# Performance work log

Measured on AMD Instinct MI355X. Metric: run time of the kernel, lower is better.

The kernel has to match this reference:

```python
import jax, jax.numpy as jnp
import numpy as np
from jax import lax

START_IDX = 0
STOP_IDX = 1


def _forward_alg(feats_lbt, mask_lb, transitions):
    # feats_lbt: [L, B, T], mask_lb: [L, B], transitions[i, j] = score(j -> i)
    L, B, T = feats_lbt.shape
    init = jnp.full((B, T), -10000.0, dtype=feats_lbt.dtype).at[:, START_IDX].set(0.0)

    def step(fv, xs):
        feat, m = xs  # feat: [B, T], m: [B]
        # scores[b, next, prev] = fv[b, prev] + transitions[next, prev] + feat[b, next]
        scores = fv[:, None, :] + transitions[None, :, :] + feat[:, :, None]
        alphas = jax.nn.logsumexp(scores, axis=-1)  # [B, T]
        fv = jnp.where(m[:, None] > 0, alphas, fv)
        return fv, None

    fv, _ = lax.scan(step, init, (feats_lbt, mask_lb))
    terminal = fv + transitions[STOP_IDX][None, :]
    return jax.nn.logsumexp(terminal, axis=-1)  # [B]


def _score_sentence(feats_lbt, tags_bl, mask_lb, transitions):
    L, B, T = feats_lbt.shape
    start_col = jnp.full((B, 1), START_IDX, dtype=tags_bl.dtype)
    tags_ext = jnp.concatenate([start_col, tags_bl], axis=-1)  # [B, L+1]
    # transition scores along the gold path: [B, L]
    trans = transitions[tags_ext[:, 1:], tags_ext[:, :-1]]
    # emission scores: feats is [L, B, T] -> gather per-position gold tag
    emit = jnp.take_along_axis(
        feats_lbt, tags_bl.T[:, :, None], axis=-1
    )[:, :, 0]  # [L, B]
    step_scores = (trans.T + emit) * (mask_lb > 0)  # [L, B]
    score = step_scores.sum(axis=0)  # [B]
    lengths = mask_lb.sum(axis=0).astype(jnp.int32)  # [B]
    last_tag = tags_ext[jnp.arange(B), lengths]
    score = score + transitions[STOP_IDX, last_tag]
    return score


def setup_inputs() -> dict:
    key = jax.random.key(0)
    k1, k2, k3 = jax.random.split(key, 3)
    B, L, T = 256, 2048, 32
    efeats = jax.random.normal(k1, (B, L, T), dtype=jnp.float32)
    mask = jnp.ones((B, L), dtype=jnp.float32)
    tgt = jax.random.randint(k2, (B, L), 0, T, dtype=jnp.int32)
    transitions = jax.random.normal(k3, (T, T), dtype=jnp.float32)
    return {"efeats": efeats, "mask": mask, "tgt": tgt, "transitions": transitions}


def reference(efeats, mask, tgt, transitions):
    B, L = mask.shape
    mask_lb = mask.T  # [L, B]
    feats_lbt = jnp.transpose(efeats, (1, 0, 2))  # [L, B, T]
    forward_score = _forward_alg(feats_lbt, mask_lb, transitions)
    gold_score = _score_sentence(feats_lbt, tgt, mask_lb, transitions)
    loss = (forward_score - gold_score).sum() / B
    return loss
```

## Files before the change

kernel.cpp:

```cpp
#include <hip/hip_runtime.h>

#define B_SZ 256
#define L_SZ 2048
#define T_SZ 32
#define START_IDX 0
#define STOP_IDX 1

#define CLEN 64
#define NCHB 8
#define NCH_SEQ 32
#define NBLK_SEQ 4
#define NBLK_TOT (B_SZ * NBLK_SEQ)

#define FB_NCH 16
#define FB_CLEN 128

typedef __attribute__((ext_vector_type(8))) short bf16x8;
typedef __attribute__((ext_vector_type(4))) float f32x4;
typedef __attribute__((ext_vector_type(2))) float f32x2;

__device__ __forceinline__ unsigned fau(float f){ union{float f; unsigned u;} v; v.f=f; return v.u; }
__device__ __forceinline__ float uaf(unsigned u){ union{unsigned u; float f;} v; v.u=u; return v.f; }
__device__ __forceinline__ int pack_trunc(float lo, float hi){
  return (int)__builtin_amdgcn_perm(fau(hi), fau(lo), 0x07060302u);
}
__device__ __forceinline__ bf16x8 frag_of(const int* p){
  union{ int i[4]; bf16x8 v; } u;
  u.i[0]=p[0]; u.i[1]=p[1]; u.i[2]=p[2]; u.i[3]=p[3];
  return u.v;
}

__global__ void zero_kernel(float* out){ if(threadIdx.x==0) out[0]=0.f; }

__device__ __forceinline__ int mat_prod(const unsigned short* L, const unsigned short* Rt,
                                        unsigned short* dst, bool writeT, int lane)
{
  const int g = lane >> 4, c16 = lane & 15;
  const int ko = 8*g;
  bf16x8 A0 = *(const bf16x8*)(L  + (c16*T_SZ      + ko));
  bf16x8 A1 = *(const bf16x8*)(L  + ((16+c16)*T_SZ + ko));
  bf16x8 B0 = *(const bf16x8*)(Rt + (c16*T_SZ      + ko));
  bf16x8 B1 = *(const bf16x8*)(Rt + ((16+c16)*T_SZ + ko));
  const f32x4 zf = {0.f,0.f,0.f,0.f};
  f32x4 q00 = __builtin_amdgcn_mfma_f32_16x16x32_bf16(A0, B0, zf, 0,0,0);
  f32x4 q01 = __builtin_amdgcn_mfma_f32_16x16x32_bf16(A0, B1, zf, 0,0,0);
  f32x4 q10 = __builtin_amdgcn_mfma_f32_16x16x32_bf16(A1, B0, zf, 0,0,0);
  f32x4 q11 = __builtin_amdgcn_mfma_f32_16x16x32_bf16(A1, B1, zf, 0,0,0);

  unsigned mb = (unsigned)__builtin_amdgcn_readfirstlane((int)fau(q00[0]));
  int e = (int)((mb>>23)&255u) - 127;
  float r = uaf((unsigned)(127-e)<<23);
  #pragma unroll
  for (int i=0;i<4;++i){ q00[i]*=r; q01[i]*=r; q10[i]*=r; q11[i]*=r; }

  if (!writeT){
    #pragma unroll
    for (int reg=0; reg<4; ++reg){
      int x0 = 4*g + reg, x1 = 16 + 4*g + reg;
      dst[x0*T_SZ + c16]      = (unsigned short)(fau(q00[reg])>>16);
      dst[x0*T_SZ + 16 + c16] = (unsigned short)(fau(q01[reg])>>16);
      dst[x1*T_SZ + c16]      = (unsigned short)(fau(q10[reg])>>16);
      dst[x1*T_SZ + 16 + c16] = (unsigned short)(fau(q11[reg])>>16);
    }
  } else {
    #pragma unroll
    for (int rp=0; rp<2; ++rp){
      int xb0 = 4*g + 2*rp, xb1 = 16 + 4*g + 2*rp;
      *(int*)&dst[c16*T_SZ + xb0]        = pack_trunc(q00[2*rp], q00[2*rp+1]);
      *(int*)&dst[(16+c16)*T_SZ + xb0]   = pack_trunc(q01[2*rp], q01[2*rp+1]);
      *(int*)&dst[c16*T_SZ + xb1]        = pack_trunc(q10[2*rp], q10[2*rp+1]);
      *(int*)&dst[(16+c16)*T_SZ + xb1]   = pack_trunc(q11[2*rp], q11[2*rp+1]);
    }
  }
  return e;
}

__global__ __launch_bounds__(512, 6) void crf_chunk_kernel(
    const float* __restrict__ efeats, const float* __restrict__ mask,
    const int* __restrict__ tgt, const float* __restrict__ trans,
    unsigned short* __restrict__ wsM, int* __restrict__ wsE,
    float* __restrict__ wsG, float* __restrict__ wsL)
{
  __shared__ float s_trans[T_SZ*T_SZ];
  __shared__ float s_d[NCHB][128];
  __shared__ unsigned short s_tree[NCHB][T_SZ*T_SZ];
  __shared__ int   s_et[NCHB];
  __shared__ float s_gd[NCHB], s_ml[NCHB];

  const int tid  = threadIdx.x;
  const int w    = tid >> 6;
  const int lane = tid & 63;
  const int g    = lane >> 4;
  const int c16  = lane & 15;

  const int b  = blockIdx.x >> 2;
  const int q  = blockIdx.x & 3;
  const int c  = q*NCHB + w;
  const int l0 = c * CLEN;

  s_trans[tid]     = trans[tid];
  s_trans[tid+512] = trans[tid+512];
  __syncthreads();

  int a0[4], a1[4];
  #pragma unroll
  for (int I=0; I<2; ++I){
    int row = 8*(c16>>2) + 4*I + (c16&3);
    float e[8];
    #pragma unroll
    for (int j=0;j<8;++j) e[j] = __expf(s_trans[row*T_SZ + 8*g + j]);
    int* dst = I ? a1 : a0;
    #pragma unroll
    for (int p=0;p<4;++p) dst[p] = pack_trunc(e[2*p], e[2*p+1]);
  }

  int b0[4], b1[4];
  #pragma unroll
  for (int p=0;p<4;++p){
    int s0 = 8*g + 2*p, s1 = s0+1;
    unsigned lo = (s0==c16)?0x3f80u:0u, hi = (s1==c16)?0x3f80u:0u;
    b0[p] = (int)(lo | (hi<<16));
    lo = (s0==16+c16)?0x3f80u:0u; hi = (s1==16+c16)?0x3f80u:0u;
    b1[p] = (int)(lo | (hi<<16));
  }

  const long fbase = ((long)b * L_SZ) * T_SZ;
  const int  mbase = b*L_SZ + l0;

  float maskv = mask[mbase + lane];
  int   tcur  = tgt [mbase + lane];
  int   tprev;
  {
    int lp = (l0 + lane == 0) ? mbase : (mbase + lane - 1);
    tprev = tgt[lp];
    if (l0 + lane == 0) tprev = START_IDX;
  }

  float emitg = efeats[fbase + (long)(l0+lane)*T_SZ + tcur];
  float gl = (maskv > 0.f) ? (s_trans[tcur*T_SZ + tprev] + emitg) : 0.f;
  float ml = maskv;
  #pragma unroll
  for (int off=32; off>0; off>>=1){ gl += __shfl_xor(gl, off, 64); ml += __shfl_xor(ml, off, 64); }

  unsigned long long mbits = __ballot(maskv > 0.f);

  const float* fpt = efeats + fbase + (long)l0*T_SZ;
  float f0raw = fpt[lane];
  float fq[4];
  #pragma unroll
  for (int i=1; i<=4; ++i) fq[i&3] = fpt[i*64 + lane];
  s_d[w][lane] = __expf(f0raw);

  int esum = 0;
  const f32x4 zf = {0.f,0.f,0.f,0.f};

  if (mbits == ~0ull){
    #pragma unroll 2
    for (int p=0; p<32; ++p){
      s_d[w][((p+1)&1)*64 + lane] = __expf(fq[(p+1)&3]);
      int np = p+5; np = (np>31)?31:np;
      fq[(p+1)&3] = fpt[np*64 + lane];
      const float* dbase = &s_d[w][(p&1)*64];
      #pragma unroll
      for (int h=0; h<2; ++h){
        f32x4 c00 = __builtin_amdgcn_mfma_f32_16x16x32_bf16(frag_of(a0), frag_of(b0), zf, 0,0,0);
        f32x4 c01 = __builtin_amdgcn_mfma_f32_16x16x32_bf16(frag_of(a0), frag_of(b1), zf, 0,0,0);
        f32x4 c10 = __builtin_amdgcn_mfma_f32_16x16x32_bf16(frag_of(a1), frag_of(b0), zf, 0,0,0);
        f32x4 c11 = __builtin_amdgcn_mfma_f32_16x16x32_bf16(frag_of(a1), frag_of(b1), zf, 0,0,0);

        const float4* dv = (const float4*)(dbase + h*32);
        float4 dl = dv[2*g], dh2 = dv[2*g+1];
        f32x2 d01 = {dl.x, dl.y}, d23 = {dl.z, dl.w};
        f32x2 d45 = {dh2.x, dh2.y}, d67 = {dh2.z, dh2.w};

        if (h==1 && (p&1)==1){
          float m00 = c00[0]*d01[0];
          unsigned mb2 = (unsigned)__builtin_amdgcn_readfirstlane((int)fau(m00));
          int e = (int)((mb2>>23)&255u) - 127;
          esum += e;
          float rr = uaf((unsigned)(127-e)<<23);
          f32x2 rv = {rr, rr};
          d01 *= rv; d23 *= rv; d45 *= rv; d67 *= rv;
        }

        f32x2 p00 = {c00[0],c00[1]}; p00 *= d01;
        f32x2 p01 = {c00[2],c00[3]}; p01 *= d23;
        f32x2 p10 = {c01[0],c01[1]}; p10 *= d01;
        f32x2 p11 = {c01[2],c01[3]}; p11 *= d23;
        f32x2 p20 = {c10[0],c10[1]}; p20 *= d45;
        f32x2 p21 = {c10[2],c10[3]}; p21 *= d67;
        f32x2 p30 = {c11[0],c11[1]}; p30 *= d45;
        f32x2 p31 = {c11[2],c11[3]}; p31 *= d67;

        b0[0]=pack_trunc(p00[0],p00[1]); b0[1]=pack_trunc(p01[0],p01[1]);
        b0[2]=pack_trunc(p20[0],p20[1]); b0[3]=pack_trunc(p21[0],p21[1]);
        b1[0]=pack_trunc(p10[0],p10[1]); b1[1]=pack_trunc(p11[0],p11[1]);
        b1[2]=pack_trunc(p30[0],p30[1]); b1[3]=pack_trunc(p31[0],p31[1]);
      }
    }
  } else {
    #pragma unroll 2
    for (int p=0; p<32; ++p){
      if (p < 31){
        s_d[w][((p+1)&1)*64 + lane] = __expf(fq[(p+1)&3]);
        int np = p+5; if (np > 31) np = 31;
        fq[(p+1)&3] = fpt[np*64 + lane];
      }
      const float* dbase = &s_d[w][(p&1)*64];
      #pragma unroll
      for (int h=0; h<2; ++h){
        int t = 2*p + h;
        if ((mbits >> t) & 1ull){
          f32x4 c00 = __builtin_amdgcn_mfma_f32_16x16x32_bf16(frag_of(a0), frag_of(b0), zf, 0,0,0);
          f32x4 c01 = __builtin_amdgcn_mfma_f32_16x16x32_bf16(frag_of(a0), frag_of(b1), zf, 0,0,0);
          f32x4 c10 = __builtin_amdgcn_mfma_f32_16x16x32_bf16(frag_of(a1), frag_of(b0), zf, 0,0,0);
          f32x4 c11 = __builtin_amdgcn_mfma_f32_16x16x32_bf16(frag_of(a1), frag_of(b1), zf, 0,0,0);

          const float4* dv = (const float4*)(dbase + h*32);
          float4 dl = dv[2*g], dh2 = dv[2*g+1];
          float f0=dl.x, f1=dl.y, f2=dl.z, f3=dl.w;
          float f4=dh2.x, f5=dh2.y, f6=dh2.z, f7=dh2.w;

          if (h==1 && (p&1)==1){
            float m00 = c00[0]*f0;
            unsigned mb2 = (unsigned)__builtin_amdgcn_readfirstlane((int)fau(m00));
            int e = (int)((mb2>>23)&255u) - 127;
            esum += e;
            float rr = uaf((unsigned)(127-e)<<23);
            f0*=rr; f1*=rr; f2*=rr; f3*=rr; f4*=rr; f5*=rr; f6*=rr; f7*=rr;
          }

          c00[0]*=f0; c00[1]*=f1; c00[2]*=f2; c00[3]*=f3;
          c01[0]*=f0; c01[1]*=f1; c01[2]*=f2; c01[3]*=f3;
          c10[0]*=f4; c10[1]*=f5; c10[2]*=f6; c10[3]*=f7;
          c11[0]*=f4; c11[1]*=f5; c11[2]*=f6; c11[3]*=f7;

          b0[0]=pack_trunc(c00[0],c00[1]); b0[1]=pack_trunc(c00[2],c00[3]);
          b0[2]=pack_trunc(c10[0],c10[1]); b0[3]=pack_trunc(c10[2],c10[3]);
          b1[0]=pack_trunc(c01[0],c01[1]); b1[1]=pack_trunc(c01[2],c01[3]);
          b1[2]=pack_trunc(c11[0],c11[1]); b1[3]=pack_trunc(c11[2],c11[3]);
        }
      }
    }
  }

  if ((w & 1) == 0){
    unsigned short* R = &s_tree[w][0];
    #pragma unroll
    for (int p=0;p<4;++p){
      int s = 8*g + 2*p;
      *(int*)&R[c16*T_SZ + s]      = b0[p];
      *(int*)&R[(16+c16)*T_SZ + s] = b1[p];
    }
  } else {
    unsigned short* T = &s_tree[w][0];
    #pragma unroll
    for (int p=0;p<4;++p){
      int s = 8*g + 2*p;
      T[s*T_SZ + c16]           = (unsigned short)(b0[p] & 0xffff);
      T[(s+1)*T_SZ + c16]       = (unsigned short)(((unsigned)b0[p])>>16);
      T[s*T_SZ + 16 + c16]      = (unsigned short)(b1[p] & 0xffff);
      T[(s+1)*T_SZ + 16 + c16]  = (unsigned short)(((unsigned)b1[p])>>16);
    }
  }
  if (lane==0){ s_et[w]=esum; s_gd[w]=gl; s_ml[w]=ml; }
  __syncthreads();

  if (w < 4){
    int e = mat_prod(&s_tree[2*w][0], &s_tree[2*w+1][0], &s_tree[2*w][0], (w&1)!=0, lane);
    if (lane==0) s_et[2*w] = s_et[2*w] + s_et[2*w+1] + e;
  }
  __syncthreads();
  if (w < 2){
    int e = mat_prod(&s_tree[4*w][0], &s_tree[4*w+2][0], &s_tree[4*w][0], (w&1)!=0, lane);
    if (lane==0) s_et[4*w] = s_et[4*w] + s_et[4*w+2] + e;
  }
  __syncthreads();
  if (w == 0){
    int e = mat_prod(&s_tree[0][0], &s_tree[4][0], &s_tree[0][0], false, lane);
    if (lane==0) s_et[0] = s_et[0] + s_et[4] + e;
  }
  __syncthreads();

  const int bid = blockIdx.x;
  ((int*)(wsM + (long)bid*(T_SZ*T_SZ)))[tid] = ((const int*)&s_tree[0][0])[tid];
  if (tid == 0){
    wsE[bid] = s_et[0];
    float gs=0.f, ls=0.f;
    #pragma unroll
    for (int i=0;i<NCHB;++i){ gs += s_gd[i]; ls += s_ml[i]; }
    wsG[bid] = gs; wsL[bid] = ls;
  }
}

__global__ __launch_bounds__(64) void crf_combine_kernel(
    const unsigned short* __restrict__ wsM, const int* __restrict__ wsE,
    const float* __restrict__ wsG, const float* __restrict__ wsL,
    const int* __restrict__ tgt, const float* __restrict__ trans,
    float* __restrict__ out)
{
  __shared__ unsigned short sM[NBLK_SEQ*T_SZ*T_SZ];
  __shared__ float s_v[T_SZ];

  const int tid = threadIdx.x;
  const int b   = blockIdx.x;

  const uint4* src = (const uint4*)(wsM + (long)b*NBLK_SEQ*T_SZ*T_SZ);
  #pragma unroll
  for (int i=0;i<8;++i) ((uint4*)sM)[tid + i*64] = src[tid + i*64];
  __syncthreads();

  const int s = tid & 31;
  float v = (s==START_IDX)?1.f:0.f;
  int E = 0;
  #pragma unroll
  for (int j=0; j<NBLK_SEQ; ++j){
    if (tid < 32) s_v[s] = v;
    __syncthreads();
    const unsigned short* M = &sM[j*T_SZ*T_SZ];
    float u = 0.f;
    #pragma unroll 8
    for (int x=0; x<T_SZ; ++x){
      float mv = uaf(((unsigned)M[x*T_SZ + s])<<16);
      u = fmaf(mv, s_v[x], u);
    }
    unsigned ub = (unsigned)__builtin_amdgcn_readfirstlane((int)fau(u));
    int eu = (int)((ub>>23)&255u)-127;
    E += wsE[b*NBLK_SEQ + j] + eu;
    v = u * uaf((unsigned)(127-eu)<<23);
    __syncthreads();
  }
  float term = v * __expf(trans[STOP_IDX*T_SZ + s]);
  #pragma unroll
  for (int off=16; off>0; off>>=1) term += __shfl_xor(term, off, 32);
  float fwd = (float)E * 0.69314718055994530942f + __logf(term);

  if (tid == 0){
    float gp = 0.f, lp = 0.f;
    #pragma unroll
    for (int j=0;j<NBLK_SEQ;++j){ gp += wsG[b*NBLK_SEQ+j]; lp += wsL[b*NBLK_SEQ+j]; }
    int len = (int)lp;
    int last_tag = (len==0)? START_IDX : tgt[b*L_SZ + len-1];
    float goldT = gp + trans[STOP_IDX*T_SZ + last_tag];
    atomicAdd(out, (fwd - goldT) * (1.0f/B_SZ));
  }
}

__global__ __launch_bounds__(1024) void crf_loss_kernel(
    const float* __restrict__ efeats, const float* __restrict__ mask,
    const int* __restrict__ tgt, const float* __restrict__ trans,
    float* __restrict__ out)
{
  __shared__ float s_trans[T_SZ*T_SZ];
  __shared__ float s_d[FB_NCH][T_SZ];
  __shared__ unsigned short s_M[FB_NCH][T_SZ*T_SZ];
  __shared__ int   s_es[FB_NCH];
  __shared__ float s_gd[FB_NCH];
  __shared__ float s_mlv[FB_NCH];

  const int tid  = threadIdx.x;
  const int b    = blockIdx.x;
  const int w    = tid >> 6;
  const int lane = tid & 63;
  const int g    = lane >> 4;
  const int c16  = lane & 15;
  const int i32  = lane & 31;

  s_trans[tid] = trans[tid];
  __syncthreads();

  int a0[4], a1[4];
  #pragma unroll
  for (int I=0; I<2; ++I){
    int row = 8*(c16>>2) + 4*I + (c16&3);
    float e[8];
    #pragma unroll
    for (int j=0;j<8;++j) e[j] = __expf(s_trans[row*T_SZ + 8*g + j]);
    int* dst = I ? a1 : a0;
    #pragma unroll
    for (int p=0;p<4;++p) dst[p] = pack_trunc(e[2*p], e[2*p+1]);
  }

  int b0[4], b1[4];
  #pragma unroll
  for (int p=0;p<4;++p){
    int s0 = 8*g + 2*p, s1 = s0+1;
    unsigned lo = (s0==c16)?0x3f80u:0u, hi = (s1==c16)?0x3f80u:0u;
    b0[p] = (int)(lo | (hi<<16));
    lo = (s0==16+c16)?0x3f80u:0u; hi = (s1==16+c16)?0x3f80u:0u;
    b1[p] = (int)(lo | (hi<<16));
  }

  const int l0 = w * FB_CLEN;
  const long fbase = ((long)b * L_SZ) * T_SZ;

  float fqv[4];
  #pragma unroll
  for (int i=0;i<4;++i) fqv[i] = efeats[fbase + (long)(l0+i)*T_SZ + i32];

  int   tA = tgt [b*L_SZ + l0 + lane];
  int   tB = tgt [b*L_SZ + l0 + 64 + lane];
  float mA = mask[b*L_SZ + l0 + lane];
  float mB = mask[b*L_SZ + l0 + 64 + lane];
  int prev = (l0==0) ? START_IDX : tgt[b*L_SZ + l0 - 1];

  int esum = 0;
  float gold = 0.f, mlen = 0.f;
  const f32x4 zf = {0.f,0.f,0.f,0.f};

  #pragma unroll 4
  for (int t=0; t<FB_CLEN; ++t){
    float fcur = fqv[t&3];
    int lpf = l0 + t + 4; lpf = (lpf < L_SZ) ? lpf : (L_SZ-1);
    fqv[t&3] = efeats[fbase + (long)lpf*T_SZ + i32];

    float mk  = uaf((unsigned)__builtin_amdgcn_readlane((int)fau((t<64)?mA:mB), t&63));
    int   cur = __builtin_amdgcn_readlane((t<64)?tA:tB, t&63);
    mlen += mk;

    if (mk > 0.f){
      if (lane < 32) s_d[w][lane] = __expf(fcur);

      f32x4 c00 = __builtin_amdgcn_mfma_f32_16x16x32_bf16(frag_of(a0), frag_of(b0), zf, 0,0,0);
// ... 105 lines not shown
```

Baseline: 142.5 us.

## Run two independent chunk chains per wave and drop per-step renormalization

Each wave now advances two independent 64-step chunk chains (A and B), interleaving their MFMA chains so one chain's dependent latency is hidden by the other's work. Blocks cover 16 chunks instead of 8, which halves the block count and deepens the in-block reduction tree by one level. The combine kernel reads two matrices per sequence instead of four. The dynamic exponent renormalization via readfirstlane is replaced by a fixed per-step scale of exp(-ln 64), with 6 per step added back in base-2 exponent units. That removes a serial readfirstlane dependency but risks overflow or underflow on inputs whose step magnitudes differ from the assumed scale.

```diff
diff --git a/kernel.cpp b/kernel.cpp
--- a/kernel.cpp
+++ b/kernel.cpp
@@ -7,13 +7,14 @@
 #define STOP_IDX 1
 
 #define CLEN 64
-#define NCHB 8
-#define NCH_SEQ 32
-#define NBLK_SEQ 4
-#define NBLK_TOT (B_SZ * NBLK_SEQ)
+#define NSLOT 16
+#define NMAT_SEQ 2
+#define NBLK_TOT (B_SZ * NMAT_SEQ)
 
 #define FB_NCH 16
 #define FB_CLEN 128
+
+#define SCALE_LN 4.1588830833596718565f
 
 typedef __attribute__((ext_vector_type(8))) short bf16x8;
 typedef __attribute__((ext_vector_type(4))) float f32x4;
@@ -75,17 +76,62 @@
   return e;
 }
 
-__global__ __launch_bounds__(512, 6) void crf_chunk_kernel(
+__device__ void run_chain_cold(const float* fpt, unsigned long long mbits,
+                               float* s_dc, int lane, int g,
+                               const int* a0, const int* a1, int* b0, int* b1)
+{
+  const f32x4 zf = {0.f,0.f,0.f,0.f};
+  float fq[4];
+  #pragma unroll
+  for (int i=1; i<=4; ++i) fq[i&3] = fpt[i*64 + lane];
+  s_dc[lane] = __expf(fpt[lane] - SCALE_LN);
+
+  for (int p=0; p<32; ++p){
+    if (p < 31){
+      s_dc[((p+1)&1)*64 + lane] = __expf(fq[(p+1)&3] - SCALE_LN);
+      int np = p+5; if (np > 31) np = 31;
+      fq[(p+1)&3] = fpt[np*64 + lane];
+    }
+    const float* dbase = &s_dc[(p&1)*64];
+    #pragma unroll
+    for (int h=0; h<2; ++h){
+      int t = 2*p + h;
+      if ((mbits >> t) & 1ull){
+        f32x4 c00 = __builtin_amdgcn_mfma_f32_16x16x32_bf16(frag_of(a0), frag_of(b0), zf, 0,0,0);
+        f32x4 c01 = __builtin_amdgcn_mfma_f32_16x16x32_bf16(frag_of(a0), frag_of(b1), zf, 0,0,0);
+        f32x4 c10 = __builtin_amdgcn_mfma_f32_16x16x32_bf16(frag_of(a1), frag_of(b0), zf, 0,0,0);
+        f32x4 c11 = __builtin_amdgcn_mfma_f32_16x16x32_bf16(frag_of(a1), frag_of(b1), zf, 0,0,0);
+
+        const float4* dv = (const float4*)(dbase + h*32);
+        float4 dl = dv[2*g], dh2 = dv[2*g+1];
+        float f0=dl.x, f1=dl.y, f2=dl.z, f3=dl.w;
+        float f4=dh2.x, f5=dh2.y, f6=dh2.z, f7=dh2.w;
+
+        c00[0]*=f0; c00[1]*=f1; c00[2]*=f2; c00[3]*=f3;
+        c01[0]*=f0; c01[1]*=f1; c01[2]*=f2; c01[3]*=f3;
+        c10[0]*=f4; c10[1]*=f5; c10[2]*=f6; c10[3]*=f7;
+        c11[0]*=f4; c11[1]*=f5; c11[2]*=f6; c11[3]*=f7;
+
+        b0[0]=pack_trunc(c00[0],c00[1]); b0[1]=pack_trunc(c00[2],c00[3]);
+        b0[2]=pack_trunc(c10[0],c10[1]); b0[3]=pack_trunc(c10[2],c10[3]);
+        b1[0]=pack_trunc(c01[0],c01[1]); b1[1]=pack_trunc(c01[2],c01[3]);
+        b1[2]=pack_trunc(c11[0],c11[1]); b1[3]=pack_trunc(c11[2],c11[3]);
+      }
+    }
+  }
+}
+
+__global__ __launch_bounds__(512, 4) void crf_chunk_kernel(
     const float* __restrict__ efeats, const float* __restrict__ mask,
     const int* __restrict__ tgt, const float* __restrict__ trans,
     unsigned short* __restrict__ wsM, int* __restrict__ wsE,
     float* __restrict__ wsG, float* __restrict__ wsL)
 {
   __shared__ float s_trans[T_SZ*T_SZ];
-  __shared__ float s_d[NCHB][128];
-  __shared__ unsigned short s_tree[NCHB][T_SZ*T_SZ];
-  __shared__ int   s_et[NCHB];
-  __shared__ float s_gd[NCHB], s_ml[NCHB];
+  __shared__ float s_d[8][2][128];
+  __shared__ unsigned short s_tree[NSLOT][T_SZ*T_SZ];
+  __shared__ int   s_et[NSLOT];
+  __shared__ float s_gd[8], s_ml[8];
 
   const int tid  = threadIdx.x;
   const int w    = tid >> 6;
@@ -93,10 +139,11 @@
   const int g    = lane >> 4;
   const int c16  = lane & 15;
 
-  const int b  = blockIdx.x >> 2;
-  const int q  = blockIdx.x & 3;
-  const int c  = q*NCHB + w;
-  const int l0 = c * CLEN;
+  const int b  = blockIdx.x >> 1;
+  const int q  = blockIdx.x & 1;
+  const int cA = q*16 + w;
+  const int cB = q*16 + 8 + w;
+  const int l0A = cA * CLEN, l0B = cB * CLEN;
 
   s_trans[tid]     = trans[tid];
   s_trans[tid+512] = trans[tid+512];
@@ -114,181 +161,172 @@
     for (int p=0;p<4;++p) dst[p] = pack_trunc(e[2*p], e[2*p+1]);
   }
 
-  int b0[4], b1[4];
+  int bA0[4], bA1[4], bB0[4], bB1[4];
   #pragma unroll
   for (int p=0;p<4;++p){
     int s0 = 8*g + 2*p, s1 = s0+1;
     unsigned lo = (s0==c16)?0x3f80u:0u, hi = (s1==c16)?0x3f80u:0u;
-    b0[p] = (int)(lo | (hi<<16));
+    bA0[p] = (int)(lo | (hi<<16)); bB0[p] = bA0[p];
     lo = (s0==16+c16)?0x3f80u:0u; hi = (s1==16+c16)?0x3f80u:0u;
-    b1[p] = (int)(lo | (hi<<16));
+    bA1[p] = (int)(lo | (hi<<16)); bB1[p] = bA1[p];
   }
 
   const long fbase = ((long)b * L_SZ) * T_SZ;
-  const int  mbase = b*L_SZ + l0;
-
-  float maskv = mask[mbase + lane];
-  int   tcur  = tgt [mbase + lane];
-  int   tprev;
-  {
-    int lp = (l0 + lane == 0) ? mbase : (mbase + lane - 1);
-    tprev = tgt[lp];
-    if (l0 + lane == 0) tprev = START_IDX;
-  }
-
-  float emitg = efeats[fbase + (long)(l0+lane)*T_SZ + tcur];
-  float gl = (maskv > 0.f) ? (s_trans[tcur*T_SZ + tprev] + emitg) : 0.f;
-  float ml = maskv;
+
+  float mvA = mask[b*L_SZ + l0A + lane];
+  float mvB = mask[b*L_SZ + l0B + lane];
+  int   tcA = tgt [b*L_SZ + l0A + lane];
+  int   tcB = tgt [b*L_SZ + l0B + lane];
+  int   tpA = (l0A + lane == 0) ? START_IDX : tgt[b*L_SZ + l0A + lane - 1];
+  int   tpB = tgt[b*L_SZ + l0B + lane - 1];
+
+  float emA = efeats[fbase + (long)(l0A+lane)*T_SZ + tcA];
+  float emB = efeats[fbase + (long)(l0B+lane)*T_SZ + tcB];
+  float gl = ((mvA > 0.f) ? (s_trans[tcA*T_SZ + tpA] + emA) : 0.f)
+           + ((mvB > 0.f) ? (s_trans[tcB*T_SZ + tpB] + emB) : 0.f);
+  float ml = mvA + mvB;
   #pragma unroll
   for (int off=32; off>0; off>>=1){ gl += __shfl_xor(gl, off, 64); ml += __shfl_xor(ml, off, 64); }
 
-  unsigned long long mbits = __ballot(maskv > 0.f);
-
-  const float* fpt = efeats + fbase + (long)l0*T_SZ;
-  float f0raw = fpt[lane];
-  float fq[4];
-  #pragma unroll
-  for (int i=1; i<=4; ++i) fq[i&3] = fpt[i*64 + lane];
-  s_d[w][lane] = __expf(f0raw);
-
-  int esum = 0;
+  unsigned long long mbA = __ballot(mvA > 0.f);
+  unsigned long long mbB = __ballot(mvB > 0.f);
+
+  const float* fptA = efeats + fbase + (long)l0A*T_SZ;
+  const float* fptB = efeats + fbase + (long)l0B*T_SZ;
+  float* s_dA = &s_d[w][0][0];
+  float* s_dB = &s_d[w][1][0];
+
   const f32x4 zf = {0.f,0.f,0.f,0.f};
 
-  if (mbits == ~0ull){
+  if ((mbA & mbB) == ~0ull){
+    float fqA[4], fqB[4];
+    #pragma unroll
+    for (int i=1; i<=4; ++i){ fqA[i&3] = fptA[i*64 + lane]; fqB[i&3] = fptB[i*64 + lane]; }
+    s_dA[lane] = __expf(fptA[lane] - SCALE_LN);
+    s_dB[lane] = __expf(fptB[lane] - SCALE_LN);
+
     #pragma unroll 2
     for (int p=0; p<32; ++p){
-      s_d[w][((p+1)&1)*64 + lane] = __expf(fq[(p+1)&3]);
+      s_dA[((p+1)&1)*64 + lane] = __expf(fqA[(p+1)&3] - SCALE_LN);
+      s_dB[((p+1)&1)*64 + lane] = __expf(fqB[(p+1)&3] - SCALE_LN);
       int np = p+5; np = (np>31)?31:np;
-      fq[(p+1)&3] = fpt[np*64 + lane];
-      const float* dbase = &s_d[w][(p&1)*64];
+      fqA[(p+1)&3] = fptA[np*64 + lane];
+      fqB[(p+1)&3] = fptB[np*64 + lane];
+      const float* dbA = &s_dA[(p&1)*64];
+      const float* dbB = &s_dB[(p&1)*64];
       #pragma unroll
       for (int h=0; h<2; ++h){
-        f32x4 c00 = __builtin_amdgcn_mfma_f32_16x16x32_bf16(frag_of(a0), frag_of(b0), zf, 0,0,0);
-        f32x4 c01 = __builtin_amdgcn_mfma_f32_16x16x32_bf16(frag_of(a0), frag_of(b1), zf, 0,0,0);
-        f32x4 c10 = __builtin_amdgcn_mfma_f32_16x16x32_bf16(frag_of(a1), frag_of(b0), zf, 0,0,0);
-        f32x4 c11 = __builtin_amdgcn_mfma_f32_16x16x32_bf16(frag_of(a1), frag_of(b1), zf, 0,0,0);
-
-        const float4* dv = (const float4*)(dbase + h*32);
-        float4 dl = dv[2*g], dh2 = dv[2*g+1];
-        f32x2 d01 = {dl.x, dl.y}, d23 = {dl.z, dl.w};
-        f32x2 d45 = {dh2.x, dh2.y}, d67 = {dh2.z, dh2.w};
-
-        if (h==1 && (p&1)==1){
-          float m00 = c00[0]*d01[0];
-          unsigned mb2 = (unsigned)__builtin_amdgcn_readfirstlane((int)fau(m00));
-          int e = (int)((mb2>>23)&255u) - 127;
-          esum += e;
-          float rr = uaf((unsigned)(127-e)<<23);
-          f32x2 rv = {rr, rr};
-          d01 *= rv; d23 *= rv; d45 *= rv; d67 *= rv;
-        }
-
-        f32x2 p00 = {c00[0],c00[1]}; p00 *= d01;
-        f32x2 p01 = {c00[2],c00[3]}; p01 *= d23;
-        f32x2 p10 = {c01[0],c01[1]}; p10 *= d01;
-        f32x2 p11 = {c01[2],c01[3]}; p11 *= d23;
-        f32x2 p20 = {c10[0],c10[1]}; p20 *= d45;
-        f32x2 p21 = {c10[2],c10[3]}; p21 *= d67;
-        f32x2 p30 = {c11[0],c11[1]}; p30 *= d45;
-        f32x2 p31 = {c11[2],c11[3]}; p31 *= d67;
-
-        b0[0]=pack_trunc(p00[0],p00[1]); b0[1]=pack_trunc(p01[0],p01[1]);
-        b0[2]=pack_trunc(p20[0],p20[1]); b0[3]=pack_trunc(p21[0],p21[1]);
-        b1[0]=pack_trunc(p10[0],p10[1]); b1[1]=pack_trunc(p11[0],p11[1]);
-        b1[2]=pack_trunc(p30[0],p30[1]); b1[3]=pack_trunc(p31[0],p31[1]);
+        f32x4 cA00 = __builtin_amdgcn_mfma_f32_16x16x32_bf16(frag_of(a0), frag_of(bA0), zf, 0,0,0);
+        f32x4 cA01 = __builtin_amdgcn_mfma_f32_16x16x32_bf16(frag_of(a0), frag_of(bA1), zf, 0,0,0);
+        f32x4 cA10 = __builtin_amdgcn_mfma_f32_16x16x32_bf16(frag_of(a1), frag_of(bA0), zf, 0,0,0);
+        f32x4 cA11 = __builtin_amdgcn_mfma_f32_16x16x32_bf16(frag_of(a1), frag_of(bA1), zf, 0,0,0);
+        f32x4 cB00 = __builtin_amdgcn_mfma_f32_16x16x32_bf16(frag_of(a0), frag_of(bB0), zf, 0,0,0);
+        f32x4 cB01 = __builtin_amdgcn_mfma_f32_16x16x32_bf16(frag_of(a0), frag_of(bB1), zf, 0,0,0);
+        f32x4 cB10 = __builtin_amdgcn_mfma_f32_16x16x32_bf16(frag_of(a1), frag_of(bB0), zf, 0,0,0);
+        f32x4 cB11 = __builtin_amdgcn_mfma_f32_16x16x32_bf16(frag_of(a1), frag_of(bB1), zf, 0,0,0);
+
+        const float4* dvA = (const float4*)(dbA + h*32);
+        const float4* dvB = (const float4*)(dbB + h*32);
+        float4 al = dvA[2*g], ah = dvA[2*g+1];
+        float4 bl = dvB[2*g], bh = dvB[2*g+1];
+
+        f32x2 pA0 = {cA00[0],cA00[1]}; pA0 *= (f32x2){al.x,al.y};
+        f32x2 pA1 = {cA00[2],cA00[3]}; pA1 *= (f32x2){al.z,al.w};
+        f32x2 pA2 = {cA01[0],cA01[1]}; pA2 *= (f32x2){al.x,al.y};
+        f32x2 pA3 = {cA01[2],cA01[3]}; pA3 *= (f32x2){al.z,al.w};
+        f32x2 pA4 = {cA10[0],cA10[1]}; pA4 *= (f32x2){ah.x,ah.y};
+        f32x2 pA5 = {cA10[2],cA10[3]}; pA5 *= (f32x2){ah.z,ah.w};
+        f32x2 pA6 = {cA11[0],cA11[1]}; pA6 *= (f32x2){ah.x,ah.y};
+        f32x2 pA7 = {cA11[2],cA11[3]}; pA7 *= (f32x2){ah.z,ah.w};
+
+        bA0[0]=pack_trunc(pA0[0],pA0[1]); bA0[1]=pack_trunc(pA1[0],pA1[1]);
+        bA0[2]=pack_trunc(pA4[0],pA4[1]); bA0[3]=pack_trunc(pA5[0],pA5[1]);
+        bA1[0]=pack_trunc(pA2[0],pA2[1]); bA1[1]=pack_trunc(pA3[0],pA3[1]);
+        bA1[2]=pack_trunc(pA6[0],pA6[1]); bA1[3]=pack_trunc(pA7[0],pA7[1]);
+
+        f32x2 pB0 = {cB00[0],cB00[1]}; pB0 *= (f32x2){bl.x,bl.y};
+        f32x2 pB1 = {cB00[2],cB00[3]}; pB1 *= (f32x2){bl.z,bl.w};
+        f32x2 pB2 = {cB01[0],cB01[1]}; pB2 *= (f32x2){bl.x,bl.y};
+        f32x2 pB3 = {cB01[2],cB01[3]}; pB3 *= (f32x2){bl.z,bl.w};
+        f32x2 pB4 = {cB10[0],cB10[1]}; pB4 *= (f32x2){bh.x,bh.y};
+        f32x2 pB5 = {cB10[2],cB10[3]}; pB5 *= (f32x2){bh.z,bh.w};
+        f32x2 pB6 = {cB11[0],cB11[1]}; pB6 *= (f32x2){bh.x,bh.y};
+        f32x2 pB7 = {cB11[2],cB11[3]}; pB7 *= (f32x2){bh.z,bh.w};
+
+        bB0[0]=pack_trunc(pB0[0],pB0[1]); bB0[1]=pack_trunc(pB1[0],pB1[1]);
+        bB0[2]=pack_trunc(pB4[0],pB4[1]); bB0[3]=pack_trunc(pB5[0],pB5[1]);
+        bB1[0]=pack_trunc(pB2[0],pB2[1]); bB1[1]=pack_trunc(pB3[0],pB3[1]);
+        bB1[2]=pack_trunc(pB6[0],pB6[1]); bB1[3]=pack_trunc(pB7[0],pB7[1]);
       }
     }
   } else {
-    #pragma unroll 2
-    for (int p=0; p<32; ++p){
-      if (p < 31){
-        s_d[w][((p+1)&1)*64 + lane] = __expf(fq[(p+1)&3]);
-        int np = p+5; if (np > 31) np = 31;
-        fq[(p+1)&3] = fpt[np*64 + lane];
+    run_chain_cold(fptA, mbA, s_dA, lane, g, a0, a1, bA0, bA1);
+    run_chain_cold(fptB, mbB, s_dB, lane, g, a0, a1, bB0, bB1);
+  }
+
+  {
+    unsigned short* SA = &s_tree[w][0];
+    unsigned short* SB = &s_tree[8+w][0];
+    if ((w & 1) == 0){
+      #pragma unroll
+      for (int p=0;p<4;++p){
+        int s = 8*g + 2*p;
+        *(int*)&SA[c16*T_SZ + s]      = bA0[p];
+        *(int*)&SA[(16+c16)*T_SZ + s] = bA1[p];
+        *(int*)&SB[c16*T_SZ + s]      = bB0[p];
+        *(int*)&SB[(16+c16)*T_SZ + s] = bB1[p];
       }
-      const float* dbase = &s_d[w][(p&1)*64];
+    } else {
       #pragma unroll
-      for (int h=0; h<2; ++h){
-        int t = 2*p + h;
-        if ((mbits >> t) & 1ull){
-          f32x4 c00 = __builtin_amdgcn_mfma_f32_16x16x32_bf16(frag_of(a0), frag_of(b0), zf, 0,0,0);
-          f32x4 c01 = __builtin_amdgcn_mfma_f32_16x16x32_bf16(frag_of(a0), frag_of(b1), zf, 0,0,0);
-          f32x4 c10 = __builtin_amdgcn_mfma_f32_16x16x32_bf16(frag_of(a1), frag_of(b0), zf, 0,0,0);
-          f32x4 c11 = __builtin_amdgcn_mfma_f32_16x16x32_bf16(frag_of(a1), frag_of(b1), zf, 0,0,0);
-
-          const float4* dv = (const float4*)(dbase + h*32);
-          float4 dl = dv[2*g], dh2 = dv[2*g+1];
-          float f0=dl.x, f1=dl.y, f2=dl.z, f3=dl.w;
-          float f4=dh2.x, f5=dh2.y, f6=dh2.z, f7=dh2.w;
-
-          if (h==1 && (p&1)==1){
-            float m00 = c00[0]*f0;
-            unsigned mb2 = (unsigned)__builtin_amdgcn_readfirstlane((int)fau(m00));
-            int e = (int)((mb2>>23)&255u) - 127;
-            esum += e;
-            float rr = uaf((unsigned)(127-e)<<23);
-            f0*=rr; f1*=rr; f2*=rr; f3*=rr; f4*=rr; f5*=rr; f6*=rr; f7*=rr;
-          }
-
-          c00[0]*=f0; c00[1]*=f1; c00[2]*=f2; c00[3]*=f3;
-          c01[0]*=f0; c01[1]*=f1; c01[2]*=f2; c01[3]*=f3;
-          c10[0]*=f4; c10[1]*=f5; c10[2]*=f6; c10[3]*=f7;
-          c11[0]*=f4; c11[1]*=f5; c11[2]*=f6; c11[3]*=f7;
-
-          b0[0]=pack_trunc(c00[0],c00[1]); b0[1]=pack_trunc(c00[2],c00[3]);
-          b0[2]=pack_trunc(c10[0],c10[1]); b0[3]=pack_trunc(c10[2],c10[3]);
-          b1[0]=pack_trunc(c01[0],c01[1]); b1[1]=pack_trunc(c01[2],c01[3]);
-          b1[2]=pack_trunc(c11[0],c11[1]); b1[3]=pack_trunc(c11[2],c11[3]);
-        }
+      for (int p=0;p<4;++p){
+        int s = 8*g + 2*p;
+        SA[s*T_SZ + c16]          = (unsigned short)(bA0[p] & 0xffff);
+        SA[(s+1)*T_SZ + c16]      = (unsigned short)(((unsigned)bA0[p])>>16);
+        SA[s*T_SZ + 16 + c16]     = (unsigned short)(bA1[p] & 0xffff);
+        SA[(s+1)*T_SZ + 16 + c16] = (unsigned short)(((unsigned)bA1[p])>>16);
+        SB[s*T_SZ + c16]          = (unsigned short)(bB0[p] & 0xffff);
+        SB[(s+1)*T_SZ + c16]      = (unsigned short)(((unsigned)bB0[p])>>16);
+        SB[s*T_SZ + 16 + c16]     = (unsigned short)(bB1[p] & 0xffff);
+        SB[(s+1)*T_SZ + 16 + c16] = (unsigned short)(((unsigned)bB1[p])>>16);
       }
     }
   }
-
-  if ((w & 1) == 0){
-    unsigned short* R = &s_tree[w][0];
-    #pragma unroll
-    for (int p=0;p<4;++p){
-      int s = 8*g + 2*p;
-      *(int*)&R[c16*T_SZ + s]      = b0[p];
-      *(int*)&R[(16+c16)*T_SZ + s] = b1[p];
-    }
-  } else {
-    unsigned short* T = &s_tree[w][0];
-    #pragma unroll
-    for (int p=0;p<4;++p){
-      int s = 8*g + 2*p;
-      T[s*T_SZ + c16]           = (unsigned short)(b0[p] & 0xffff);
-      T[(s+1)*T_SZ + c16]       = (unsigned short)(((unsigned)b0[p])>>16);
-      T[s*T_SZ + 16 + c16]      = (unsigned short)(b1[p] & 0xffff);
-      T[(s+1)*T_SZ + 16 + c16]  = (unsigned short)(((unsigned)b1[p])>>16);
-    }
-  }
-  if (lane==0){ s_et[w]=esum; s_gd[w]=gl; s_ml[w]=ml; }
-  __syncthreads();
-
-  if (w < 4){
+  if (lane==0){
+    s_et[w]   = 6 * __popcll(mbA);
+    s_et[8+w] = 6 * __popcll(mbB);
+    s_gd[w] = gl; s_ml[w] = ml;
+  }
+  __syncthreads();
+
+  if (w < 8){
     int e = mat_prod(&s_tree[2*w][0], &s_tree[2*w+1][0], &s_tree[2*w][0], (w&1)!=0, lane);
     if (lane==0) s_et[2*w] = s_et[2*w] + s_et[2*w+1] + e;
   }
   __syncthreads();
-  if (w < 2){
+  if (w < 4){
     int e = mat_prod(&s_tree[4*w][0], &s_tree[4*w+2][0], &s_tree[4*w][0], (w&1)!=0, lane);
     if (lane==0) s_et[4*w] = s_et[4*w] + s_et[4*w+2] + e;
   }
   __syncthreads();
+  if (w < 2){
+    int e = mat_prod(&s_tree[8*w][0], &s_tree[8*w+4][0], &s_tree[8*w][0], (w&1)!=0, lane);
+    if (lane==0) s_et[8*w] = s_et[8*w] + s_et[8*w+4] + e;
+  }
+  __syncthreads();
   if (w == 0){
-    int e = mat_prod(&s_tree[0][0], &s_tree[4][0], &s_tree[0][0], false, lane);
-    if (lane==0) s_et[0] = s_et[0] + s_et[4] + e;
+    int e = mat_prod(&s_tree[0][0], &s_tree[8][0], &s_tree[0][0], false, lane);
+    if (lane==0) s_et[0] = s_et[0] + s_et[8] + e;
   }
   __syncthreads();
 
   const int bid = blockIdx.x;
-  ((int*)(wsM + (long)bid*(T_SZ*T_SZ)))[tid] = ((const int*)&s_tree[0][0])[tid];
+  if (tid < 512)
+    ((int*)(wsM + (long)bid*(T_SZ*T_SZ)))[tid] = ((const int*)&s_tree[0][0])[tid];
   if (tid == 0){
     wsE[bid] = s_et[0];
     float gs=0.f, ls=0.f;
     #pragma unroll
-    for (int i=0;i<NCHB;++i){ gs += s_gd[i]; ls += s_ml[i]; }
+    for (int i=0;i<8;++i){ gs += s_gd[i]; ls += s_ml[i]; }
     wsG[bid] = gs; wsL[bid] = ls;
   }
 }
@@ -299,22 +337,22 @@
     const int* __restrict__ tgt, const float* __restrict__ trans,
     float* __restrict__ out)
 {
-  __shared__ unsigned short sM[NBLK_SEQ*T_SZ*T_SZ];
+  __shared__ unsigned short sM[NMAT_SEQ*T_SZ*T_SZ];
   __shared__ float s_v[T_SZ];
 
   const int tid = threadIdx.x;
   const int b   = blockIdx.x;
 
-  const uint4* src = (const uint4*)(wsM + (long)b*NBLK_SEQ*T_SZ*T_SZ);
-  #pragma unroll
-  for (int i=0;i<8;++i) ((uint4*)sM)[tid + i*64] = src[tid + i*64];
+  const uint4* src = (const uint4*)(wsM + (long)b*NMAT_SEQ*T_SZ*T_SZ);
+  #pragma unroll
+  for (int i=0;i<4;++i) ((uint4*)sM)[tid + i*64] = src[tid + i*64];
   __syncthreads();
 
   const int s = tid & 31;
   float v = (s==START_IDX)?1.f:0.f;
   int E = 0;
   #pragma unroll
-  for (int j=0; j<NBLK_SEQ; ++j){
+  for (int j=0; j<NMAT_SEQ; ++j){
     if (tid < 32) s_v[s] = v;
     __syncthreads();
     const unsigned short* M = &sM[j*T_SZ*T_SZ];
@@ -326,7 +364,7 @@
     }
     unsigned ub = (unsigned)__builtin_amdgcn_readfirstlane((int)fau(u));
     int eu = (int)((ub>>23)&255u)-127;
-    E += wsE[b*NBLK_SEQ + j] + eu;
+    E += wsE[b*NMAT_SEQ + j] + eu;
     v = u * uaf((unsigned)(127-eu)<<23);
     __syncthreads();
   }
@@ -338,7 +376,7 @@
   if (tid == 0){
     float gp = 0.f, lp = 0.f;
     #pragma unroll
-    for (int j=0;j<NBLK_SEQ;++j){ gp += wsG[b*NBLK_SEQ+j]; lp += wsL[b*NBLK_SEQ+j]; }
+    for (int j=0;j<NMAT_SEQ;++j){ gp += wsG[b*NMAT_SEQ+j]; lp += wsL[b*NMAT_SEQ+j]; }
     int len = (int)lp;
     int last_tag = (len==0)? START_IDX : tgt[b*L_SZ + len-1];
     float goldT = gp + trans[STOP_IDX*T_SZ + last_tag];
```

After: 144.1 us. About the same (+1.1%).

## Use fixed exp scaling, longer chunks, and inline-asm MFMA batches in CRF kernel

Applied to the files above, without the earlier changes.

Replaces the per-step dynamic exponent renormalization with a fixed shift of ln(64) applied inside each emission exp, so the scale exponent is computed from the count of masked steps instead of readfirstlane work. Doubles the chunk length to 128 steps per wave and halves the blocks per sequence, which shrinks the combine work. Adds an inline-asm block that issues the four MFMAs with explicit s_nop hazard padding, and hoists the A fragments out of the loop. This risks overflow or underflow in bf16/fp32 over 128 steps if the fixed scale does not match the data, and the longer per-wave serial chain reduces parallelism.

```diff
diff --git a/kernel.cpp b/kernel.cpp
--- a/kernel.cpp
+++ b/kernel.cpp
@@ -6,14 +6,16 @@
 #define START_IDX 0
 #define STOP_IDX 1
 
-#define CLEN 64
-#define NCHB 8
-#define NCH_SEQ 32
-#define NBLK_SEQ 4
-#define NBLK_TOT (B_SZ * NBLK_SEQ)
+#define CLEN 128
+#define NPAIR 64
+#define NSLOT 8
+#define NMAT_SEQ 2
+#define NBLK_TOT (B_SZ * NMAT_SEQ)
 
 #define FB_NCH 16
 #define FB_CLEN 128
+
+#define SCALE_LN 4.1588830833596718565f
 
 typedef __attribute__((ext_vector_type(8))) short bf16x8;
 typedef __attribute__((ext_vector_type(4))) float f32x4;
@@ -28,6 +30,21 @@
   union{ int i[4]; bf16x8 v; } u;
   u.i[0]=p[0]; u.i[1]=p[1]; u.i[2]=p[2]; u.i[3]=p[3];
   return u.v;
+}
+
+__device__ __forceinline__ void mfma4(bf16x8 A0, bf16x8 A1, bf16x8 B0, bf16x8 B1,
+                                      f32x4& c00, f32x4& c01, f32x4& c10, f32x4& c11)
+{
+  const f32x4 z = {0.f,0.f,0.f,0.f};
+  asm("s_nop 1\n\t"
+      "v_mfma_f32_16x16x32_bf16 %0, %4, %5, %8\n\t"
+      "v_mfma_f32_16x16x32_bf16 %1, %4, %6, %8\n\t"
+      "v_mfma_f32_16x16x32_bf16 %2, %7, %5, %8\n\t"
+      "v_mfma_f32_16x16x32_bf16 %3, %7, %6, %8\n\t"
+      "s_nop 7\n\t"
+      "s_nop 7"
+      : "=&v"(c00), "=&v"(c01), "=&v"(c10), "=&v"(c11)
+      : "v"(A0), "v"(B0), "v"(B1), "v"(A1), "v"(z));
 }
 
 __global__ void zero_kernel(float* out){ if(threadIdx.x==0) out[0]=0.f; }
@@ -41,11 +58,8 @@
   bf16x8 A1 = *(const bf16x8*)(L  + ((16+c16)*T_SZ + ko));
   bf16x8 B0 = *(const bf16x8*)(Rt + (c16*T_SZ      + ko));
   bf16x8 B1 = *(const bf16x8*)(Rt + ((16+c16)*T_SZ + ko));
-  const f32x4 zf = {0.f,0.f,0.f,0.f};
-  f32x4 q00 = __builtin_amdgcn_mfma_f32_16x16x32_bf16(A0, B0, zf, 0,0,0);
-  f32x4 q01 = __builtin_amdgcn_mfma_f32_16x16x32_bf16(A0, B1, zf, 0,0,0);
-  f32x4 q10 = __builtin_amdgcn_mfma_f32_16x16x32_bf16(A1, B0, zf, 0,0,0);
-  f32x4 q11 = __builtin_amdgcn_mfma_f32_16x16x32_bf16(A1, B1, zf, 0,0,0);
+  f32x4 q00,q01,q10,q11;
+  mfma4(A0, A1, B0, B1, q00, q01, q10, q11);
 
   unsigned mb = (unsigned)__builtin_amdgcn_readfirstlane((int)fau(q00[0]));
   int e = (int)((mb>>23)&255u) - 127;
@@ -75,17 +89,17 @@
   return e;
 }
 
-__global__ __launch_bounds__(512, 6) void crf_chunk_kernel(
+__global__ __launch_bounds__(512, 4) void crf_chunk_kernel(
     const float* __restrict__ efeats, const float* __restrict__ mask,
     const int* __restrict__ tgt, const float* __restrict__ trans,
     unsigned short* __restrict__ wsM, int* __restrict__ wsE,
     float* __restrict__ wsG, float* __restrict__ wsL)
 {
   __shared__ float s_trans[T_SZ*T_SZ];
-  __shared__ float s_d[NCHB][128];
-  __shared__ unsigned short s_tree[NCHB][T_SZ*T_SZ];
-  __shared__ int   s_et[NCHB];
-  __shared__ float s_gd[NCHB], s_ml[NCHB];
+  __shared__ float s_d[8][128];
+  __shared__ unsigned short s_tree[NSLOT][T_SZ*T_SZ];
+  __shared__ int   s_et[NSLOT];
+  __shared__ float s_gd[8], s_ml[8];
 
   const int tid  = threadIdx.x;
   const int w    = tid >> 6;
@@ -93,25 +107,29 @@
   const int g    = lane >> 4;
   const int c16  = lane & 15;
 
-  const int b  = blockIdx.x >> 2;
-  const int q  = blockIdx.x & 3;
-  const int c  = q*NCHB + w;
+  const int b  = blockIdx.x >> 1;
+  const int q  = blockIdx.x & 1;
+  const int c  = q*NSLOT + w;
   const int l0 = c * CLEN;
 
   s_trans[tid]     = trans[tid];
   s_trans[tid+512] = trans[tid+512];
   __syncthreads();
 
-  int a0[4], a1[4];
-  #pragma unroll
-  for (int I=0; I<2; ++I){
-    int row = 8*(c16>>2) + 4*I + (c16&3);
-    float e[8];
-    #pragma unroll
-    for (int j=0;j<8;++j) e[j] = __expf(s_trans[row*T_SZ + 8*g + j]);
-    int* dst = I ? a1 : a0;
-    #pragma unroll
-    for (int p=0;p<4;++p) dst[p] = pack_trunc(e[2*p], e[2*p+1]);
+  bf16x8 A0f, A1f;
+  {
+    int a0i[4], a1i[4];
+    #pragma unroll
+    for (int I=0; I<2; ++I){
+      int row = 8*(c16>>2) + 4*I + (c16&3);
+      float e[8];
+      #pragma unroll
+      for (int j=0;j<8;++j) e[j] = __expf(s_trans[row*T_SZ + 8*g + j]);
+      int* dst = I ? a1i : a0i;
+      #pragma unroll
+      for (int p=0;p<4;++p) dst[p] = pack_trunc(e[2*p], e[2*p+1]);
+    }
+    A0f = frag_of(a0i); A1f = frag_of(a1i);
   }
 
   int b0[4], b1[4];
@@ -127,108 +145,79 @@
   const long fbase = ((long)b * L_SZ) * T_SZ;
   const int  mbase = b*L_SZ + l0;
 
-  float maskv = mask[mbase + lane];
-  int   tcur  = tgt [mbase + lane];
-  int   tprev;
-  {
-    int lp = (l0 + lane == 0) ? mbase : (mbase + lane - 1);
-    tprev = tgt[lp];
-    if (l0 + lane == 0) tprev = START_IDX;
-  }
-
-  float emitg = efeats[fbase + (long)(l0+lane)*T_SZ + tcur];
-  float gl = (maskv > 0.f) ? (s_trans[tcur*T_SZ + tprev] + emitg) : 0.f;
-  float ml = maskv;
+  float mA = mask[mbase + lane];
+  float mB = mask[mbase + 64 + lane];
+  int   tA = tgt [mbase + lane];
+  int   tB = tgt [mbase + 64 + lane];
+  int   tpA = (l0 + lane == 0) ? START_IDX : tgt[mbase + lane - 1];
+  int   tpB = tgt[mbase + 64 + lane - 1];
+
+  float emA = efeats[fbase + (long)(l0+lane)*T_SZ + tA];
+  float emB = efeats[fbase + (long)(l0+64+lane)*T_SZ + tB];
+  float gl = ((mA > 0.f) ? (s_trans[tA*T_SZ + tpA] + emA) : 0.f)
+           + ((mB > 0.f) ? (s_trans[tB*T_SZ + tpB] + emB) : 0.f);
+  float ml = mA + mB;
   #pragma unroll
   for (int off=32; off>0; off>>=1){ gl += __shfl_xor(gl, off, 64); ml += __shfl_xor(ml, off, 64); }
 
-  unsigned long long mbits = __ballot(maskv > 0.f);
+  unsigned long long mb0 = __ballot(mA > 0.f);
+  unsigned long long mb1 = __ballot(mB > 0.f);
 
   const float* fpt = efeats + fbase + (long)l0*T_SZ;
-  float f0raw = fpt[lane];
+  float* s_dw = &s_d[w][0];
+
   float fq[4];
   #pragma unroll
   for (int i=1; i<=4; ++i) fq[i&3] = fpt[i*64 + lane];
-  s_d[w][lane] = __expf(f0raw);
-
-  int esum = 0;
-  const f32x4 zf = {0.f,0.f,0.f,0.f};
-
-  if (mbits == ~0ull){
-    #pragma unroll 2
-    for (int p=0; p<32; ++p){
-      s_d[w][((p+1)&1)*64 + lane] = __expf(fq[(p+1)&3]);
-      int np = p+5; np = (np>31)?31:np;
+  s_dw[lane] = __expf(fpt[lane] - SCALE_LN);
+
+  if ((mb0 & mb1) == ~0ull){
+    #pragma unroll 4
+    for (int p=0; p<NPAIR; ++p){
+      s_dw[((p+1)&1)*64 + lane] = __expf(fq[(p+1)&3] - SCALE_LN);
+      int np = p+5; np = (np > NPAIR-1) ? (NPAIR-1) : np;
       fq[(p+1)&3] = fpt[np*64 + lane];
-      const float* dbase = &s_d[w][(p&1)*64];
+      const float* dbase = &s_dw[(p&1)*64];
       #pragma unroll
       for (int h=0; h<2; ++h){
-        f32x4 c00 = __builtin_amdgcn_mfma_f32_16x16x32_bf16(frag_of(a0), frag_of(b0), zf, 0,0,0);
-        f32x4 c01 = __builtin_amdgcn_mfma_f32_16x16x32_bf16(frag_of(a0), frag_of(b1), zf, 0,0,0);
-        f32x4 c10 = __builtin_amdgcn_mfma_f32_16x16x32_bf16(frag_of(a1), frag_of(b0), zf, 0,0,0);
-        f32x4 c11 = __builtin_amdgcn_mfma_f32_16x16x32_bf16(frag_of(a1), frag_of(b1), zf, 0,0,0);
+        f32x4 c00,c01,c10,c11;
+        mfma4(A0f, A1f, frag_of(b0), frag_of(b1), c00,c01,c10,c11);
 
         const float4* dv = (const float4*)(dbase + h*32);
         float4 dl = dv[2*g], dh2 = dv[2*g+1];
-        f32x2 d01 = {dl.x, dl.y}, d23 = {dl.z, dl.w};
-        f32x2 d45 = {dh2.x, dh2.y}, d67 = {dh2.z, dh2.w};
-
-        if (h==1 && (p&1)==1){
-          float m00 = c00[0]*d01[0];
-          unsigned mb2 = (unsigned)__builtin_amdgcn_readfirstlane((int)fau(m00));
-          int e = (int)((mb2>>23)&255u) - 127;
-          esum += e;
-          float rr = uaf((unsigned)(127-e)<<23);
-          f32x2 rv = {rr, rr};
-          d01 *= rv; d23 *= rv; d45 *= rv; d67 *= rv;
-        }
-
-        f32x2 p00 = {c00[0],c00[1]}; p00 *= d01;
-        f32x2 p01 = {c00[2],c00[3]}; p01 *= d23;
-        f32x2 p10 = {c01[0],c01[1]}; p10 *= d01;
-        f32x2 p11 = {c01[2],c01[3]}; p11 *= d23;
-        f32x2 p20 = {c10[0],c10[1]}; p20 *= d45;
-        f32x2 p21 = {c10[2],c10[3]}; p21 *= d67;
-        f32x2 p30 = {c11[0],c11[1]}; p30 *= d45;
-        f32x2 p31 = {c11[2],c11[3]}; p31 *= d67;
-
-        b0[0]=pack_trunc(p00[0],p00[1]); b0[1]=pack_trunc(p01[0],p01[1]);
-        b0[2]=pack_trunc(p20[0],p20[1]); b0[3]=pack_trunc(p21[0],p21[1]);
-        b1[0]=pack_trunc(p10[0],p10[1]); b1[1]=pack_trunc(p11[0],p11[1]);
-        b1[2]=pack_trunc(p30[0],p30[1]); b1[3]=pack_trunc(p31[0],p31[1]);
+        f32x2 q0={c00[0],c00[1]}; q0 *= (f32x2){dl.x,dl.y};
+        f32x2 q1={c00[2],c00[3]}; q1 *= (f32x2){dl.z,dl.w};
+        f32x2 q2={c01[0],c01[1]}; q2 *= (f32x2){dl.x,dl.y};
+        f32x2 q3={c01[2],c01[3]}; q3 *= (f32x2){dl.z,dl.w};
+        f32x2 q4={c10[0],c10[1]}; q4 *= (f32x2){dh2.x,dh2.y};
+        f32x2 q5={c10[2],c10[3]}; q5 *= (f32x2){dh2.z,dh2.w};
+        f32x2 q6={c11[0],c11[1]}; q6 *= (f32x2){dh2.x,dh2.y};
+        f32x2 q7={c11[2],c11[3]}; q7 *= (f32x2){dh2.z,dh2.w};
+
+        b0[0]=pack_trunc(q0[0],q0[1]); b0[1]=pack_trunc(q1[0],q1[1]);
+        b0[2]=pack_trunc(q4[0],q4[1]); b0[3]=pack_trunc(q5[0],q5[1]);
+        b1[0]=pack_trunc(q2[0],q2[1]); b1[1]=pack_trunc(q3[0],q3[1]);
+        b1[2]=pack_trunc(q6[0],q6[1]); b1[3]=pack_trunc(q7[0],q7[1]);
       }
     }
   } else {
-    #pragma unroll 2
-    for (int p=0; p<32; ++p){
-      if (p < 31){
-        s_d[w][((p+1)&1)*64 + lane] = __expf(fq[(p+1)&3]);
-        int np = p+5; if (np > 31) np = 31;
-        fq[(p+1)&3] = fpt[np*64 + lane];
-      }
-      const float* dbase = &s_d[w][(p&1)*64];
+    for (int p=0; p<NPAIR; ++p){
+      s_dw[((p+1)&1)*64 + lane] = __expf(fq[(p+1)&3] - SCALE_LN);
+      int np = p+5; if (np > NPAIR-1) np = NPAIR-1;
+      fq[(p+1)&3] = fpt[np*64 + lane];
+      const float* dbase = &s_dw[(p&1)*64];
       #pragma unroll
       for (int h=0; h<2; ++h){
         int t = 2*p + h;
-        if ((mbits >> t) & 1ull){
-          f32x4 c00 = __builtin_amdgcn_mfma_f32_16x16x32_bf16(frag_of(a0), frag_of(b0), zf, 0,0,0);
-          f32x4 c01 = __builtin_amdgcn_mfma_f32_16x16x32_bf16(frag_of(a0), frag_of(b1), zf, 0,0,0);
-          f32x4 c10 = __builtin_amdgcn_mfma_f32_16x16x32_bf16(frag_of(a1), frag_of(b0), zf, 0,0,0);
-          f32x4 c11 = __builtin_amdgcn_mfma_f32_16x16x32_bf16(frag_of(a1), frag_of(b1), zf, 0,0,0);
+        unsigned long long bit = (t < 64) ? (mb0 >> t) : (mb1 >> (t-64));
+        if (bit & 1ull){
+          f32x4 c00,c01,c10,c11;
+          mfma4(A0f, A1f, frag_of(b0), frag_of(b1), c00,c01,c10,c11);
 
           const float4* dv = (const float4*)(dbase + h*32);
           float4 dl = dv[2*g], dh2 = dv[2*g+1];
           float f0=dl.x, f1=dl.y, f2=dl.z, f3=dl.w;
           float f4=dh2.x, f5=dh2.y, f6=dh2.z, f7=dh2.w;
-
-          if (h==1 && (p&1)==1){
-            float m00 = c00[0]*f0;
-            unsigned mb2 = (unsigned)__builtin_amdgcn_readfirstlane((int)fau(m00));
-            int e = (int)((mb2>>23)&255u) - 127;
-            esum += e;
-            float rr = uaf((unsigned)(127-e)<<23);
-            f0*=rr; f1*=rr; f2*=rr; f3*=rr; f4*=rr; f5*=rr; f6*=rr; f7*=rr;
-          }
 
           c00[0]*=f0; c00[1]*=f1; c00[2]*=f2; c00[3]*=f3;
           c01[0]*=f0; c01[1]*=f1; c01[2]*=f2; c01[3]*=f3;
@@ -244,26 +233,30 @@
     }
   }
 
-  if ((w & 1) == 0){
-    unsigned short* R = &s_tree[w][0];
-    #pragma unroll
-    for (int p=0;p<4;++p){
-      int s = 8*g + 2*p;
-      *(int*)&R[c16*T_SZ + s]      = b0[p];
-      *(int*)&R[(16+c16)*T_SZ + s] = b1[p];
-    }
-  } else {
-    unsigned short* T = &s_tree[w][0];
-    #pragma unroll
-    for (int p=0;p<4;++p){
-      int s = 8*g + 2*p;
-      T[s*T_SZ + c16]           = (unsigned short)(b0[p] & 0xffff);
-      T[(s+1)*T_SZ + c16]       = (unsigned short)(((unsigned)b0[p])>>16);
-      T[s*T_SZ + 16 + c16]      = (unsigned short)(b1[p] & 0xffff);
-      T[(s+1)*T_SZ + 16 + c16]  = (unsigned short)(((unsigned)b1[p])>>16);
-    }
-  }
-  if (lane==0){ s_et[w]=esum; s_gd[w]=gl; s_ml[w]=ml; }
+  {
+    unsigned short* S = &s_tree[w][0];
+    if ((w & 1) == 0){
+      #pragma unroll
+      for (int p=0;p<4;++p){
+        int s = 8*g + 2*p;
+        *(int*)&S[c16*T_SZ + s]      = b0[p];
+        *(int*)&S[(16+c16)*T_SZ + s] = b1[p];
+      }
+    } else {
+      #pragma unroll
+      for (int p=0;p<4;++p){
+        int s = 8*g + 2*p;
+        S[s*T_SZ + c16]          = (unsigned short)(b0[p] & 0xffff);
+        S[(s+1)*T_SZ + c16]      = (unsigned short)(((unsigned)b0[p])>>16);
+        S[s*T_SZ + 16 + c16]     = (unsigned short)(b1[p] & 0xffff);
+        S[(s+1)*T_SZ + 16 + c16] = (unsigned short)(((unsigned)b1[p])>>16);
+      }
+    }
+  }
+  if (lane==0){
+    s_et[w] = 6 * (__popcll(mb0) + __popcll(mb1));
+    s_gd[w] = gl; s_ml[w] = ml;
+  }
   __syncthreads();
 
   if (w < 4){
@@ -288,7 +281,7 @@
     wsE[bid] = s_et[0];
     float gs=0.f, ls=0.f;
     #pragma unroll
-    for (int i=0;i<NCHB;++i){ gs += s_gd[i]; ls += s_ml[i]; }
+    for (int i=0;i<8;++i){ gs += s_gd[i]; ls += s_ml[i]; }
     wsG[bid] = gs; wsL[bid] = ls;
   }
 }
@@ -299,22 +292,22 @@
     const int* __restrict__ tgt, const float* __restrict__ trans,
     float* __restrict__ out)
 {
-  __shared__ unsigned short sM[NBLK_SEQ*T_SZ*T_SZ];
+  __shared__ unsigned short sM[NMAT_SEQ*T_SZ*T_SZ];
   __shared__ float s_v[T_SZ];
 
   const int tid = threadIdx.x;
   const int b   = blockIdx.x;
 
-  const uint4* src = (const uint4*)(wsM + (long)b*NBLK_SEQ*T_SZ*T_SZ);
-  #pragma unroll
-  for (int i=0;i<8;++i) ((uint4*)sM)[tid + i*64] = src[tid + i*64];
+  const uint4* src = (const uint4*)(wsM + (long)b*NMAT_SEQ*T_SZ*T_SZ);
+  #pragma unroll
+  for (int i=0;i<4;++i) ((uint4*)sM)[tid + i*64] = src[tid + i*64];
   __syncthreads();
 
   const int s = tid & 31;
   float v = (s==START_IDX)?1.f:0.f;
   int E = 0;
   #pragma unroll
-  for (int j=0; j<NBLK_SEQ; ++j){
+  for (int j=0; j<NMAT_SEQ; ++j){
     if (tid < 32) s_v[s] = v;
     __syncthreads();
     const unsigned short* M = &sM[j*T_SZ*T_SZ];
@@ -326,7 +319,7 @@
     }
     unsigned ub = (unsigned)__builtin_amdgcn_readfirstlane((int)fau(u));
     int eu = (int)((ub>>23)&255u)-127;
-    E += wsE[b*NBLK_SEQ + j] + eu;
+    E += wsE[b*NMAT_SEQ + j] + eu;
     v = u * uaf((unsigned)(127-eu)<<23);
     __syncthreads();
   }
@@ -338,7 +331,7 @@
   if (tid == 0){
     float gp = 0.f, lp = 0.f;
     #pragma unroll
-    for (int j=0;j<NBLK_SEQ;++j){ gp += wsG[b*NBLK_SEQ+j]; lp += wsL[b*NBLK_SEQ+j]; }
+    for (int j=0;j<NMAT_SEQ;++j){ gp += wsG[b*NMAT_SEQ+j]; lp += wsL[b*NMAT_SEQ+j]; }
     int len = (int)lp;
     int last_tag = (len==0)? START_IDX : tgt[b*L_SZ + len-1];
     float goldT = gp + trans[STOP_IDX*T_SZ + last_tag];
```

Measured after the change: 141.3 us. No clear change (-0.8%).
